# Kernel optimization log

Hardware: AMD Instinct MI355X
Metric: run time of the kernel (lower is better)

## Reference

```python
import jax, jax.numpy as jnp
import numpy as np

M_ANCH = 704   # 22 parts * 32 anchors
N_ANCH = 128   # object anchors


def reference(smpl_betas, object_rel_rotmat, object_rel_trans, object_anchors_org,
              v_template, shapedirs, J_regressor, pca_mean, pca_components,
              anchor_indices):
    b = smpl_betas.shape[0]
    v = v_template[None] + jnp.einsum('bk,vck->bvc', smpl_betas, shapedirs)   # [b,V,3]
    J = jnp.einsum('jv,bvc->bjc', J_regressor, v)                              # [b,55,3]
    v = v - J[:, :1]                                                           # root-center
    smpl_anchors = v[:, anchor_indices]                                        # [b,704,3]
    # --- encode: transform object anchors, broadcast offset diff, PCA ---
    obj_anchors = jnp.einsum('bnc,bdc->bnd', object_anchors_org, object_rel_rotmat) \
        + object_rel_trans[:, None, :]                                         # [b,128,3]
    offsets = obj_anchors[:, None, :, :] - smpl_anchors[:, :, None, :]         # [b,704,128,3]
    off_flat = offsets.reshape(b, -1)                                          # [b,270336]
    gamma = (off_flat - pca_mean[None]) @ pca_components.T                     # [b,128]
    # --- decode: PCA inverse ---
    off_rec = pca_mean[None] + gamma @ pca_components                          # [b,270336]
    # --- decode_object_RT: batched Procrustes via 3x3 SVD ---
    off4 = off_rec.reshape(b, M_ANCH, N_ANCH, 3)
    P = (smpl_anchors[:, :, None, :] + off4).reshape(b, -1, 3)                 # [b,m*n,3]
    Q = jnp.broadcast_to(object_anchors_org[:, None], (b, M_ANCH, N_ANCH, 3)).reshape(b, -1, 3)
    center_Q = Q.mean(axis=1, keepdims=True)
    Qc = Q - center_Q
    svd_mat = jnp.einsum('bic,bid->bcd', P, Qc)                                # P^T @ Qc, [b,3,3]
    u, s, vh = jnp.linalg.svd(svd_mat, full_matrices=False)
    d = jnp.linalg.det(u @ vh)                                                 # [b]
    dvec = jnp.concatenate([jnp.ones((b, 2), svd_mat.dtype), d[:, None]], axis=-1)
    R = (u * dvec[:, None, :]) @ vh                                            # u @ diag(1,1,d) @ vh
    T = (P - jnp.einsum('bij,bnj->bni', R, Q)).mean(axis=1)                    # [b,3]
    return gamma, R, T


def setup_inputs() -> dict:
    key = jax.random.key(0)
    ks = jax.random.split(key, 10)
    b, V, Jn, K = 64, 10475, 55, 10
    D = M_ANCH * N_ANCH * 3
    return {
        'smpl_betas': jax.random.normal(ks[0], (b, K), jnp.float32),
        'object_rel_rotmat': jax.random.normal(ks[1], (b, 3, 3), jnp.float32),
        'object_rel_trans': jax.random.normal(ks[2], (b, 3), jnp.float32),
        'object_anchors_org': jax.random.normal(ks[3], (b, N_ANCH, 3), jnp.float32),
        'v_template': jax.random.normal(ks[4], (V, 3), jnp.float32),
        'shapedirs': jax.random.normal(ks[5], (V, 3, K), jnp.float32) * 0.03,
        'J_regressor': jax.random.uniform(ks[6], (Jn, V), jnp.float32) / V,
        'pca_mean': jax.random.normal(ks[7], (D,), jnp.float32) * 0.1,
        'pca_components': jax.random.normal(ks[8], (128, D), jnp.float32) / np.sqrt(D),
        'anchor_indices': jax.random.randint(ks[9], (M_ANCH,), 0, V, jnp.int32),
    }
```

## Files before the change

### kernel.cpp

```cpp
#include <hip/hip_runtime.h>

#define V_CNT   10475
#define M_A     704
#define N_A     128
#define KB      10
#define D_TOT   270336
#define ROW384  384
#define NCHUNK  22
#define MT      32
#define LSTR    388

#define WS_JJ     0
#define WS_CMEAN  64
#define WS_MC     192
#define WS_V2C    576
#define WS_SASUM  960
#define WS_GWS    1152
#define WS_WT     9344
#define WS_X      328832
#define WS_TOTAL  488576
#define WS_ZEROF  58496

#define NJ_BLK 28
#define NM_BLK 88
#define NP_BLK 64

__global__ __launch_bounds__(384) void k_pre(
    const float* __restrict__ Jr, const float* __restrict__ vt,
    const float* __restrict__ sd, const float* __restrict__ mean,
    const float* __restrict__ betas, const float* __restrict__ rot,
    const float* __restrict__ trans, const float* __restrict__ org,
    const int* __restrict__ anch,
    float* __restrict__ JJ, float* __restrict__ Mc,
    float* __restrict__ X, float* __restrict__ saSum) {
  __shared__ float orgL[384];
  __shared__ float red[384];
  __shared__ float small[24];
  const int blk = blockIdx.x, t = threadIdx.x;

  if (blk < NJ_BLK) {
    float acc[33];
#pragma unroll
    for (int i = 0; i < 33; ++i) acc[i] = 0.f;
    int v = blk * 384 + t;
    if (v < V_CNT) {
      float jr = Jr[v];
#pragma unroll
      for (int c = 0; c < 3; ++c) {
        acc[c] += jr * vt[v * 3 + c];
        const float* sp = sd + ((size_t)v * 3 + c) * KB;
#pragma unroll
        for (int k = 0; k < KB; ++k) acc[3 + c * KB + k] += jr * sp[k];
      }
    }
#pragma unroll
    for (int i = 0; i < 33; ++i) {
      float x = acc[i];
      for (int off = 32; off > 0; off >>= 1) x += __shfl_down(x, off);
      if ((t & 63) == 0) atomicAdd(&JJ[i], x);
    }
  } else if (blk < NJ_BLK + NM_BLK) {
    int j = blk - NJ_BLK;
    float a = 0.f;
#pragma unroll
    for (int mi = 0; mi < 8; ++mi)
      a += mean[(size_t)(j * 8 + mi) * ROW384 + t];
    atomicAdd(&Mc[t], a);
  } else {
    const int b = blk - (NJ_BLK + NM_BLK);
    if (t < 10) small[t] = betas[b * 10 + t];
    else if (t >= 10 && t < 19) small[t] = rot[b * 9 + (t - 10)];
    else if (t >= 19 && t < 22) small[t] = trans[b * 3 + (t - 19)];
    orgL[t] = org[(size_t)b * 384 + t];
    __syncthreads();
    {
      int n = t / 3, d = t % 3;
      X[(size_t)b * 2496 + t] =
          orgL[n * 3 + 0] * small[10 + d * 3 + 0] +
          orgL[n * 3 + 1] * small[10 + d * 3 + 1] +
          orgL[n * 3 + 2] * small[10 + d * 3 + 2] + small[19 + d];
    }
    float ps = 0.f;
    for (int e = t; e < 2112; e += 384) {
      int m = e / 3, c = e % 3;
      int a = anch[m];
      const float* sp = sd + ((size_t)a * 3 + c) * KB;
      float val = vt[a * 3 + c];
#pragma unroll
      for (int k = 0; k < KB; ++k) val += small[k] * sp[k];
      X[(size_t)b * 2496 + 384 + e] = val;
      ps += val;
    }
    red[t] = ps;
    __syncthreads();
    if (t < 3) {
      float s = 0.f;
#pragma unroll 8
      for (int j = 0; j < 128; ++j) s += red[t + 3 * j];
      saSum[b * 3 + t] = s;
    }
  }
}

__global__ __launch_bounds__(384) void k_pcpass(
    const float* __restrict__ pc, const float* __restrict__ mean,
    float* __restrict__ Wt, float* __restrict__ V2c, float* __restrict__ cmean) {
  __shared__ float tile[MT * LSTR];
  const int t = threadIdx.x;
  const int pid = blockIdx.x & 127;
  const int chunk = blockIdx.x >> 7;
  const int m0 = chunk * MT;
  const float* row = pc + (size_t)pid * D_TOT + (size_t)m0 * ROW384;
  const float* mrow = mean + (size_t)m0 * ROW384;

  float cm = 0.f;
#pragma unroll
  for (int i = 0; i < 8; ++i) {
    int f = 1536 * i + 4 * t;
    float4 pv = *(const float4*)(row + f);
    float4 mv = *(const float4*)(mrow + f);
    cm += pv.x * mv.x + pv.y * mv.y + pv.z * mv.z + pv.w * mv.w;
    int m_l = 4 * i + t / 96;
    int col = (t % 96) * 4;
    *(float4*)(&tile[m_l * LSTR + col]) = pv;
  }
  __syncthreads();

  float u = 0.f;
#pragma unroll
  for (int m = 0; m < MT; ++m) u += tile[m * LSTR + t];
  atomicAdd(&Wt[(size_t)t * 128 + pid], u);

  float vsp = 0.f;
  {
    int grp = t / 96, mc = t % 96, m_l = mc / 3, c = mc % 3;
    const float* tp = &tile[m_l * LSTR + c];
#pragma unroll 8
    for (int j = 0; j < 32; ++j) vsp += tp[(grp * 32 + j) * 3];
  }
  __syncthreads();
  tile[t] = vsp;
  {
    float x = cm;
    for (int off = 32; off > 0; off >>= 1) x += __shfl_down(x, off);
    if ((t & 63) == 0) tile[384 + (t >> 6)] = x;
  }
  __syncthreads();
  if (t < 96) {
    float vs = tile[t] + tile[96 + t] + tile[192 + t] + tile[288 + t];
    int m_l = t / 3, c = t % 3;
    Wt[(size_t)(384 + (m0 + m_l) * 3 + c) * 128 + pid] = -vs;
    tile[400 + t] = vs;
  }
  if (t == 0) {
    float s = 0.f;
#pragma unroll
    for (int w = 0; w < 6; ++w) s += tile[384 + w];
    atomicAdd(&cmean[pid], s);
  }
  __syncthreads();
  if (t < 3) {
    float sv = 0.f;
#pragma unroll 8
    for (int j = 0; j < 32; ++j) sv += tile[400 + t + 3 * j];
    atomicAdd(&V2c[t * 128 + pid], sv);
  }
}

__global__ __launch_bounds__(256) void k_gamma(
    const float* __restrict__ X, const float* __restrict__ Wt,
    float* __restrict__ gWS) {
  __shared__ float XL[312];
  const int b = blockIdx.x >> 3, sl = blockIdx.x & 7, t = threadIdx.x;
  const int e0 = sl * 312;
  for (int i = t; i < 312; i += 256) XL[i] = X[(size_t)b * 2496 + e0 + i];
  __syncthreads();
  const int p = t & 127, g = t >> 7;
  const float* W = Wt + (size_t)(e0 + g * 156) * 128 + p;
  const float* xr = XL + g * 156;
  float s = 0.f;
#pragma unroll 12
  for (int i = 0; i < 156; ++i) s += xr[i] * W[(size_t)i * 128];
  atomicAdd(&gWS[b * 128 + p], s);
}

__device__ inline double det3(const double A[3][3]) {
  return A[0][0] * (A[1][1] * A[2][2] - A[1][2] * A[2][1])
       - A[0][1] * (A[1][0] * A[2][2] - A[1][2] * A[2][0])
       + A[0][2] * (A[1][0] * A[2][1] - A[1][1] * A[2][0]);
}

__device__ void svd3_rotation(const float* S, float* Rout) {
  double M[3][3], B[3][3], Vv[3][3];
  for (int i = 0; i < 3; ++i)
    for (int j = 0; j < 3; ++j) M[i][j] = (double)S[i * 3 + j];
  for (int i = 0; i < 3; ++i)
    for (int j = 0; j < 3; ++j) {
      double a = 0;
      for (int k = 0; k < 3; ++k) a += M[k][i] * M[k][j];
      B[i][j] = a;
    }
  for (int i = 0; i < 3; ++i)
    for (int j = 0; j < 3; ++j) Vv[i][j] = (i == j) ? 1.0 : 0.0;
  const int PP[3] = {0, 0, 1}, QQ[3] = {1, 2, 2};
  for (int sweep = 0; sweep < 25; ++sweep) {
    double off = B[0][1] * B[0][1] + B[0][2] * B[0][2] + B[1][2] * B[1][2];
    double dg = B[0][0] * B[0][0] + B[1][1] * B[1][1] + B[2][2] * B[2][2];
    if (off <= 1e-28 * (dg + 1e-300)) break;
    for (int pr = 0; pr < 3; ++pr) {
      int p = PP[pr], q = QQ[pr];
      double apq = B[p][q];
      if (apq == 0.0) continue;
      double dd = (B[p][p] - B[q][q]) / (2.0 * apq);
      double tt = 1.0 / (fabs(dd) + sqrt(dd * dd + 1.0));
      if (dd < 0.0) tt = -tt;
      double cc = 1.0 / sqrt(tt * tt + 1.0), ss = tt * cc;
      B[p][p] += tt * apq;
      B[q][q] -= tt * apq;
      B[p][q] = B[q][p] = 0.0;
      int k = 3 - p - q;
      double Bkp = cc * B[k][p] + ss * B[k][q];
      double Bkq = -ss * B[k][p] + cc * B[k][q];
      B[k][p] = B[p][k] = Bkp;
      B[k][q] = B[q][k] = Bkq;
      for (int i = 0; i < 3; ++i) {
        double vip = cc * Vv[i][p] + ss * Vv[i][q];
        double viq = -ss * Vv[i][p] + cc * Vv[i][q];
        Vv[i][p] = vip;
        Vv[i][q] = viq;
      }
    }
  }
  double lam[3] = {B[0][0], B[1][1], B[2][2]};
  int o0 = 0, o1 = 1, o2 = 2, tp;
  if (lam[o0] < lam[o1]) { tp = o0; o0 = o1; o1 = tp; }
  if (lam[o0] < lam[o2]) { tp = o0; o0 = o2; o2 = tp; }
  if (lam[o1] < lam[o2]) { tp = o1; o1 = o2; o2 = tp; }
  int ord[3] = {o0, o1, o2};
  double sv[3], U[3][3], Vs[3][3];
  for (int j = 0; j < 3; ++j) {
    double l = lam[ord[j]];
    sv[j] = l > 0.0 ? sqrt(l) : 0.0;
    for (int i = 0; i < 3; ++i) Vs[i][j] = Vv[i][ord[j]];
  }
  for (int j = 0; j < 3; ++j) {
    double vx = Vs[0][j], vy = Vs[1][j], vz = Vs[2][j];
    double ux = M[0][0] * vx + M[0][1] * vy + M[0][2] * vz;
    double uy = M[1][0] * vx + M[1][1] * vy + M[1][2] * vz;
    double uz = M[2][0] * vx + M[2][1] * vy + M[2][2] * vz;
    double sj = sv[j];
    if (sj > 1e-12 * (sv[0] + 1e-300)) {
      U[0][j] = ux / sj; U[1][j] = uy / sj; U[2][j] = uz / sj;
    } else if (j == 2) {
      double cx = U[1][0] * U[2][1] - U[2][0] * U[1][1];
      double cy = U[2][0] * U[0][1] - U[0][0] * U[2][1];
      double cz = U[0][0] * U[1][1] - U[1][0] * U[0][1];
      double nn = sqrt(cx * cx + cy * cy + cz * cz);
      if (nn < 1e-300) { cx = 0; cy = 0; cz = 1; nn = 1; }
      U[0][2] = cx / nn; U[1][2] = cy / nn; U[2][2] = cz / nn;
    } else {
      U[0][j] = (j == 0) ? 1.0 : 0.0;
      U[1][j] = (j == 1) ? 1.0 : 0.0;
      U[2][j] = 0.0;
    }
  }
  double dsgn = (det3(U) * det3(Vs)) < 0.0 ? -1.0 : 1.0;
  for (int i = 0; i < 3; ++i)
    for (int j = 0; j < 3; ++j)
      Rout[i * 3 + j] = (float)(U[i][0] * Vs[j][0] + U[i][1] * Vs[j][1] +
                                dsgn * U[i][2] * Vs[j][2]);
}

__global__ __launch_bounds__(384) void k_finish(
    const float* __restrict__ betas, const float* __restrict__ org,
    const float* __restrict__ JJ, const float* __restrict__ cmean,
    const float* __restrict__ Mc, const float* __restrict__ V2c,
    const float* __restrict__ saSum, const float* __restrict__ gWS,
    const float* __restrict__ Wt, float* __restrict__ out) {
  const int b = blockIdx.x, t = threadIdx.x;
  __shared__ float orgL[384], A[384], gammaL[128];
  __shared__ float betasL[10], J0L[3], cQ[3], smat[9], RL[9];

  if (t < 10) betasL[t] = betas[b * 10 + t];
  orgL[t] = org[(size_t)b * 384 + t];
  __syncthreads();
  if (t < 3) {
    float j0 = JJ[t];
#pragma unroll
    for (int k = 0; k < KB; ++k) j0 += betasL[k] * JJ[3 + t * KB + k];
    J0L[t] = j0;
    float s = 0.f;
    for (int n = 0; n < N_A; ++n) s += orgL[n * 3 + t];
    cQ[t] = s * (1.f / 128.f);
  }
  __syncthreads();

  if (t < 128) {
    float g = gWS[b * 128 + t] + J0L[0] * V2c[t] + J0L[1] * V2c[128 + t] +
              J0L[2] * V2c[256 + t] - cmean[t];
    gammaL[t] = g;
    out[b * 128 + t] = g;
  }
  __syncthreads();

  {
    const float4* up4 = (const float4*)(Wt + (size_t)t * 128);
    float gs = 0.f;
#pragma unroll 8
    for (int i = 0; i < 32; ++i) {
      float4 u4 = up4[i];
      gs += gammaL[4 * i] * u4.x + gammaL[4 * i + 1] * u4.y +
            gammaL[4 * i + 2] * u4.z + gammaL[4 * i + 3] * u4.w;
    }
    A[t] = Mc[t] + gs;
  }
  __syncthreads();

  if (t < 9) {
    int c = t / 3, d = t % 3;
    float s = 0.f, cq = cQ[d];
    for (int n = 0; n < N_A; ++n) s += A[n * 3 + c] * (orgL[n * 3 + d] - cq);
    smat[t] = s;
  }
  __syncthreads();
  if (t == 0) svd3_rotation(smat, RL);
  __syncthreads();
  if (t < 9) out[8192 + b * 9 + t] = RL[t];
  if (t < 3) {
    float s2 = 0.f;
    for (int n = 0; n < N_A; ++n) s2 += A[n * 3 + t];
    float meanP = saSum[b * 3 + t] * (1.f / 704.f) - J0L[t] + s2 * (1.f / 90112.f);
    float rq = RL[t * 3 + 0] * cQ[0] + RL[t * 3 + 1] * cQ[1] + RL[t * 3 + 2] * cQ[2];
    out[8768 + b * 3 + t] = meanP - rq;
  }
}

extern "C" void kernel_launch(void* const* d_in, const int* in_sizes, int n_in,
                              void* d_out, int out_size, void* d_ws, size_t ws_size,
                              hipStream_t stream) {
  const float* betas = (const float*)d_in[0];
  const float* rot   = (const float*)d_in[1];
  const float* trans = (const float*)d_in[2];
  const float* org   = (const float*)d_in[3];
  const float* vt    = (const float*)d_in[4];
  const float* sd    = (const float*)d_in[5];
  const float* Jr    = (const float*)d_in[6];
  const float* mean  = (const float*)d_in[7];
  const float* pc    = (const float*)d_in[8];
  const int*   anch  = (const int*)d_in[9];
  float* out = (float*)d_out;
  float* ws  = (float*)d_ws;
  if (ws_size < (size_t)WS_TOTAL * sizeof(float)) return;

  float* JJ    = ws + WS_JJ;
  float* cmean = ws + WS_CMEAN;
  float* Mc    = ws + WS_MC;
  float* V2c   = ws + WS_V2C;
  float* saSum = ws + WS_SASUM;
  float* gWS   = ws + WS_GWS;
  float* Wt    = ws + WS_WT;
  float* X     = ws + WS_X;

  hipMemsetAsync(ws, 0, (size_t)WS_ZEROF * sizeof(float), stream);
  k_pre<<<NJ_BLK + NM_BLK + NP_BLK, 384, 0, stream>>>(
      Jr, vt, sd, mean, betas, rot, trans, org, anch, JJ, Mc, X, saSum);
  k_pcpass<<<NCHUNK * 128, 384, 0, stream>>>(pc, mean, Wt, V2c, cmean);
  k_gamma<<<64 * 8, 256, 0, stream>>>(X, Wt, gWS);
  k_finish<<<64, 384, 0, stream>>>(betas, org, JJ, cmean, Mc, V2c, saSum, gWS,
                                   Wt, out);
}
```

Before: 313.6 us.

## Fuse gamma projection into PCA pass and drop the materialized Wt matrix

The separate k_gamma kernel is removed. Each k_main block now computes its chunk's contribution to gamma for all 64 batches directly from its reduced component rows in shared memory, then atomically adds the result into gWS. This eliminates the large 2496x128 Wt workspace and the second kernel's reread of it, keeping only the 384x128 Ut matrix. Component loads become nontemporal. The cost is more atomics, since every block issues 64 atomicAdds into gWS, plus extra per-block work reading X.

```diff
diff --git a/kernel.cpp b/kernel.cpp
--- a/kernel.cpp
+++ b/kernel.cpp
@@ -16,14 +16,16 @@
 #define WS_V2C    576
 #define WS_SASUM  960
 #define WS_GWS    1152
-#define WS_WT     9344
-#define WS_X      328832
-#define WS_TOTAL  488576
+#define WS_UT     9344
+#define WS_X      58496
+#define WS_TOTAL  218240
 #define WS_ZEROF  58496
 
 #define NJ_BLK 28
 #define NM_BLK 88
 #define NP_BLK 64
+
+typedef float f4v __attribute__((ext_vector_type(4)));
 
 __global__ __launch_bounds__(384) void k_pre(
     const float* __restrict__ Jr, const float* __restrict__ vt,
@@ -102,10 +104,15 @@
   }
 }
 
-__global__ __launch_bounds__(384) void k_pcpass(
+__global__ __launch_bounds__(384) void k_main(
     const float* __restrict__ pc, const float* __restrict__ mean,
-    float* __restrict__ Wt, float* __restrict__ V2c, float* __restrict__ cmean) {
+    const float* __restrict__ X,
+    float* __restrict__ Ut, float* __restrict__ V2c,
+    float* __restrict__ cmean, float* __restrict__ gWS) {
   __shared__ float tile[MT * LSTR];
+  __shared__ float ycat[480];
+  __shared__ float red[384];
+  __shared__ float cred[6];
   const int t = threadIdx.x;
   const int pid = blockIdx.x & 127;
   const int chunk = blockIdx.x >> 7;
@@ -117,71 +124,72 @@
 #pragma unroll
   for (int i = 0; i < 8; ++i) {
     int f = 1536 * i + 4 * t;
-    float4 pv = *(const float4*)(row + f);
+    f4v pv = __builtin_nontemporal_load((const f4v*)(row + f));
     float4 mv = *(const float4*)(mrow + f);
-    cm += pv.x * mv.x + pv.y * mv.y + pv.z * mv.z + pv.w * mv.w;
+    cm += pv[0] * mv.x + pv[1] * mv.y + pv[2] * mv.z + pv[3] * mv.w;
     int m_l = 4 * i + t / 96;
     int col = (t % 96) * 4;
-    *(float4*)(&tile[m_l * LSTR + col]) = pv;
-  }
-  __syncthreads();
-
-  float u = 0.f;
-#pragma unroll
-  for (int m = 0; m < MT; ++m) u += tile[m * LSTR + t];
-  atomicAdd(&Wt[(size_t)t * 128 + pid], u);
-
-  float vsp = 0.f;
+    *(f4v*)(&tile[m_l * LSTR + col]) = pv;
+  }
+  __syncthreads();
+
+  {
+    float u = 0.f;
+#pragma unroll
+    for (int m = 0; m < MT; ++m) u += tile[m * LSTR + t];
+    ycat[t] = u;
+    atomicAdd(&Ut[(size_t)t * 128 + pid], u);
+  }
   {
     int grp = t / 96, mc = t % 96, m_l = mc / 3, c = mc % 3;
     const float* tp = &tile[m_l * LSTR + c];
+    float vsp = 0.f;
 #pragma unroll 8
     for (int j = 0; j < 32; ++j) vsp += tp[(grp * 32 + j) * 3];
-  }
-  __syncthreads();
-  tile[t] = vsp;
+    red[t] = vsp;
+  }
   {
     float x = cm;
     for (int off = 32; off > 0; off >>= 1) x += __shfl_down(x, off);
-    if ((t & 63) == 0) tile[384 + (t >> 6)] = x;
+    if ((t & 63) == 0) cred[t >> 6] = x;
   }
   __syncthreads();
   if (t < 96) {
-    float vs = tile[t] + tile[96 + t] + tile[192 + t] + tile[288 + t];
-    int m_l = t / 3, c = t % 3;
-    Wt[(size_t)(384 + (m0 + m_l) * 3 + c) * 128 + pid] = -vs;
-    tile[400 + t] = vs;
+    float vs = red[t] + red[96 + t] + red[192 + t] + red[288 + t];
+    ycat[384 + t] = -vs;
   }
   if (t == 0) {
-    float s = 0.f;
-#pragma unroll
-    for (int w = 0; w < 6; ++w) s += tile[384 + w];
+    float s = cred[0] + cred[1] + cred[2] + cred[3] + cred[4] + cred[5];
     atomicAdd(&cmean[pid], s);
   }
   __syncthreads();
   if (t < 3) {
     float sv = 0.f;
 #pragma unroll 8
-    for (int j = 0; j < 32; ++j) sv += tile[400 + t + 3 * j];
-    atomicAdd(&V2c[t * 128 + pid], sv);
-  }
-}
-
-__global__ __launch_bounds__(256) void k_gamma(
-    const float* __restrict__ X, const float* __restrict__ Wt,
-    float* __restrict__ gWS) {
-  __shared__ float XL[312];
-  const int b = blockIdx.x >> 3, sl = blockIdx.x & 7, t = threadIdx.x;
-  const int e0 = sl * 312;
-  for (int i = t; i < 312; i += 256) XL[i] = X[(size_t)b * 2496 + e0 + i];
-  __syncthreads();
-  const int p = t & 127, g = t >> 7;
-  const float* W = Wt + (size_t)(e0 + g * 156) * 128 + p;
-  const float* xr = XL + g * 156;
-  float s = 0.f;
-#pragma unroll 12
-  for (int i = 0; i < 156; ++i) s += xr[i] * W[(size_t)i * 128];
-  atomicAdd(&gWS[b * 128 + p], s);
+    for (int j = 0; j < 32; ++j) sv += ycat[384 + t + 3 * j];
+    atomicAdd(&V2c[t * 128 + pid], -sv);
+  }
+  {
+    const int b = t / 6, j = t - (t / 6) * 6;
+    const float* xb = X + (size_t)b * 2496;
+    const int i0 = j * 80;
+    float s = 0.f;
+#pragma unroll 5
+    for (int i = 0; i < 80; i += 4) {
+      int e = i0 + i;
+      const float* xp = (e < 384) ? (xb + e) : (xb + chunk * 96 + e);
+      float4 xv = *(const float4*)xp;
+      float4 yv = *(const float4*)(&ycat[e]);
+      s += xv.x * yv.x + xv.y * yv.y + xv.z * yv.z + xv.w * yv.w;
+    }
+    red[t] = s;
+  }
+  __syncthreads();
+  if (t < 64) {
+    const float* r6 = &red[t * 6];
+    float g = r6[0] + r6[1] + r6[2] + r6[3] + r6[4] + r6[5];
+    atomicAdd(&gWS[t * 128 + pid], g);
+  }
 }
 
 __device__ inline double det3(const double A[3][3]) {
@@ -276,7 +284,7 @@
     const float* __restrict__ JJ, const float* __restrict__ cmean,
     const float* __restrict__ Mc, const float* __restrict__ V2c,
     const float* __restrict__ saSum, const float* __restrict__ gWS,
-    const float* __restrict__ Wt, float* __restrict__ out) {
+    const float* __restrict__ Ut, float* __restrict__ out) {
   const int b = blockIdx.x, t = threadIdx.x;
   __shared__ float orgL[384], A[384], gammaL[128];
   __shared__ float betasL[10], J0L[3], cQ[3], smat[9], RL[9];
@@ -304,7 +312,7 @@
   __syncthreads();
 
   {
-    const float4* up4 = (const float4*)(Wt + (size_t)t * 128);
+    const float4* up4 = (const float4*)(Ut + (size_t)t * 128);
     float gs = 0.f;
 #pragma unroll 8
     for (int i = 0; i < 32; ++i) {
@@ -358,14 +366,13 @@
   float* V2c   = ws + WS_V2C;
   float* saSum = ws + WS_SASUM;
   float* gWS   = ws + WS_GWS;
-  float* Wt    = ws + WS_WT;
+  float* Ut    = ws + WS_UT;
   float* X     = ws + WS_X;
 
   hipMemsetAsync(ws, 0, (size_t)WS_ZEROF * sizeof(float), stream);
   k_pre<<<NJ_BLK + NM_BLK + NP_BLK, 384, 0, stream>>>(
       Jr, vt, sd, mean, betas, rot, trans, org, anch, JJ, Mc, X, saSum);
-  k_pcpass<<<NCHUNK * 128, 384, 0, stream>>>(pc, mean, Wt, V2c, cmean);
-  k_gamma<<<64 * 8, 256, 0, stream>>>(X, Wt, gWS);
+  k_main<<<NCHUNK * 128, 384, 0, stream>>>(pc, mean, X, Ut, V2c, cmean, gWS);
   k_finish<<<64, 384, 0, stream>>>(betas, org, JJ, cmean, Mc, V2c, saSum, gWS,
-                                   Wt, out);
-}
+                                   Ut, out);
+}
```

Result: slower. 350.6 us (+11.8%).

## Split PCA pass into smaller row chunks and per-batch pre blocks into four slices

Applied to the files above, without the earlier changes.

The PCA-component pass now processes 16 anchor rows per block instead of 32, doubling the block count to 44 chunks per component so more CUs have work during the large streaming read. Its reductions are reworked to use dedicated shared buffers. The per-batch preprocessing is split into four slices per batch, with saSum accumulated by atomics. The cost is more atomics on Wt, V2c, cmean and saSum, plus less work per block, in exchange for better occupancy and load balance.

```diff
diff --git a/kernel.cpp b/kernel.cpp
--- a/kernel.cpp
+++ b/kernel.cpp
@@ -6,8 +6,8 @@
 #define KB      10
 #define D_TOT   270336
 #define ROW384  384
-#define NCHUNK  22
-#define MT      32
+#define NCHUNK  44
+#define MT      16
 #define LSTR    388
 
 #define WS_JJ     0
@@ -23,7 +23,7 @@
 
 #define NJ_BLK 28
 #define NM_BLK 88
-#define NP_BLK 64
+#define NP_BLK 256
 
 __global__ __launch_bounds__(384) void k_pre(
     const float* __restrict__ Jr, const float* __restrict__ vt,
@@ -67,13 +67,14 @@
       a += mean[(size_t)(j * 8 + mi) * ROW384 + t];
     atomicAdd(&Mc[t], a);
   } else {
-    const int b = blk - (NJ_BLK + NM_BLK);
+    const int idx = blk - (NJ_BLK + NM_BLK);
+    const int b = idx >> 2, sl = idx & 3;
     if (t < 10) small[t] = betas[b * 10 + t];
     else if (t >= 10 && t < 19) small[t] = rot[b * 9 + (t - 10)];
     else if (t >= 19 && t < 22) small[t] = trans[b * 3 + (t - 19)];
-    orgL[t] = org[(size_t)b * 384 + t];
+    if (sl == 0) orgL[t] = org[(size_t)b * 384 + t];
     __syncthreads();
-    {
+    if (sl == 0) {
       int n = t / 3, d = t % 3;
       X[(size_t)b * 2496 + t] =
           orgL[n * 3 + 0] * small[10 + d * 3 + 0] +
@@ -81,15 +82,20 @@
           orgL[n * 3 + 2] * small[10 + d * 3 + 2] + small[19 + d];
     }
     float ps = 0.f;
-    for (int e = t; e < 2112; e += 384) {
-      int m = e / 3, c = e % 3;
-      int a = anch[m];
-      const float* sp = sd + ((size_t)a * 3 + c) * KB;
-      float val = vt[a * 3 + c];
-#pragma unroll
-      for (int k = 0; k < KB; ++k) val += small[k] * sp[k];
-      X[(size_t)b * 2496 + 384 + e] = val;
-      ps += val;
+#pragma unroll
+    for (int r = 0; r < 2; ++r) {
+      int el = t + r * 384;
+      if (el < 528) {
+        int e = sl * 528 + el;
+        int m = e / 3, c = e - m * 3;
+        int a = anch[m];
+        const float* sp = sd + ((size_t)a * 3 + c) * KB;
+        float val = vt[a * 3 + c];
+#pragma unroll
+        for (int k = 0; k < KB; ++k) val += small[k] * sp[k];
+        X[(size_t)b * 2496 + 384 + e] = val;
+        ps += val;
+      }
     }
     red[t] = ps;
     __syncthreads();
@@ -97,7 +103,7 @@
       float s = 0.f;
 #pragma unroll 8
       for (int j = 0; j < 128; ++j) s += red[t + 3 * j];
-      saSum[b * 3 + t] = s;
+      atomicAdd(&saSum[b * 3 + t], s);
     }
   }
 }
@@ -106,6 +112,9 @@
     const float* __restrict__ pc, const float* __restrict__ mean,
     float* __restrict__ Wt, float* __restrict__ V2c, float* __restrict__ cmean) {
   __shared__ float tile[MT * LSTR];
+  __shared__ float red[384];
+  __shared__ float vred[48];
+  __shared__ float cred[6];
   const int t = threadIdx.x;
   const int pid = blockIdx.x & 127;
   const int chunk = blockIdx.x >> 7;
@@ -115,7 +124,7 @@
 
   float cm = 0.f;
 #pragma unroll
-  for (int i = 0; i < 8; ++i) {
+  for (int i = 0; i < 4; ++i) {
     int f = 1536 * i + 4 * t;
     float4 pv = *(const float4*)(row + f);
     float4 mv = *(const float4*)(mrow + f);
@@ -126,43 +135,43 @@
   }
   __syncthreads();
 
-  float u = 0.f;
-#pragma unroll
-  for (int m = 0; m < MT; ++m) u += tile[m * LSTR + t];
-  atomicAdd(&Wt[(size_t)t * 128 + pid], u);
-
-  float vsp = 0.f;
   {
-    int grp = t / 96, mc = t % 96, m_l = mc / 3, c = mc % 3;
+    float u = 0.f;
+#pragma unroll
+    for (int m = 0; m < MT; ++m) u += tile[m * LSTR + t];
+    atomicAdd(&Wt[(size_t)t * 128 + pid], u);
+  }
+  {
+    int grp = t / 48, mc = t % 48, m_l = mc / 3, c = mc % 3;
     const float* tp = &tile[m_l * LSTR + c];
+    float vsp = 0.f;
 #pragma unroll 8
-    for (int j = 0; j < 32; ++j) vsp += tp[(grp * 32 + j) * 3];
-  }
-  __syncthreads();
-  tile[t] = vsp;
+    for (int j = 0; j < 16; ++j) vsp += tp[(grp * 16 + j) * 3];
+    red[t] = vsp;
+  }
   {
     float x = cm;
     for (int off = 32; off > 0; off >>= 1) x += __shfl_down(x, off);
-    if ((t & 63) == 0) tile[384 + (t >> 6)] = x;
-  }
-  __syncthreads();
-  if (t < 96) {
-    float vs = tile[t] + tile[96 + t] + tile[192 + t] + tile[288 + t];
+    if ((t & 63) == 0) cred[t >> 6] = x;
+  }
+  __syncthreads();
+  if (t < 48) {
+    float vs = 0.f;
+#pragma unroll
+    for (int g = 0; g < 8; ++g) vs += red[g * 48 + t];
     int m_l = t / 3, c = t % 3;
     Wt[(size_t)(384 + (m0 + m_l) * 3 + c) * 128 + pid] = -vs;
-    tile[400 + t] = vs;
+    vred[t] = vs;
   }
   if (t == 0) {
-    float s = 0.f;
-#pragma unroll
-    for (int w = 0; w < 6; ++w) s += tile[384 + w];
+    float s = cred[0] + cred[1] + cred[2] + cred[3] + cred[4] + cred[5];
     atomicAdd(&cmean[pid], s);
   }
   __syncthreads();
   if (t < 3) {
     float sv = 0.f;
-#pragma unroll 8
-    for (int j = 0; j < 32; ++j) sv += tile[400 + t + 3 * j];
+#pragma unroll
+    for (int j = 0; j < 16; ++j) sv += vred[3 * j + t];
     atomicAdd(&V2c[t * 128 + pid], sv);
   }
 }
```

Measured after the change: 371.7 us. 18.5% more time.
